# Kernel tuning notes

Measured on AMD Instinct MI355X. Metric: run time of the kernel, lower is better.

The kernel has to match this reference:

```python
import jax, jax.numpy as jnp
import numpy as np

B, S, N, D_IN, D_OUT = 8, 512, 128, 256, 64
D_HID = D_IN // 2


def setup_inputs() -> dict:
    key = jax.random.key(0)
    ks = jax.random.split(key, 12)
    sc_in = 1.0 / np.sqrt(D_IN)
    sc_hid = 1.0 / np.sqrt(D_HID)
    return {
        "x": jax.random.normal(ks[0], (B, S, N, D_IN), jnp.float32),
        "seq_lengths": jax.random.randint(ks[1], (B,), 0, S),
        # attention1: Linear(D_in, D_hid)
        "W1": jax.random.normal(ks[2], (D_HID, D_IN), jnp.float32) * sc_in,
        "b1": jax.random.normal(ks[3], (D_HID,), jnp.float32) * sc_in,
        # weight_len: (D_hid, 1) xavier param, stored as a vector
        "w_len": jax.random.normal(ks[4], (D_HID,), jnp.float32) * sc_hid,
        # attention: Linear(D_in, D_in)
        "Wa": jax.random.normal(ks[5], (D_IN, D_IN), jnp.float32) * sc_in,
        "ba": jax.random.normal(ks[6], (D_IN,), jnp.float32) * sc_in,
        # embedding: Linear(D_in, D_in)
        "We": jax.random.normal(ks[7], (D_IN, D_IN), jnp.float32) * sc_in,
        "be": jax.random.normal(ks[8], (D_IN,), jnp.float32) * sc_in,
        # fc2: Linear(D_in, D_out)
        "Wf": jax.random.normal(ks[9], (D_OUT, D_IN), jnp.float32) * sc_in,
        "bf": jax.random.normal(ks[10], (D_OUT,), jnp.float32) * sc_in,
    }


def reference(x, seq_lengths, W1, b1, w_len, Wa, ba, We, be, Wf, bf):
    # x: (batch, seq_len, num_nodes, D_in) -- torch code transposes to
    # (num_nodes, seq_len, batch, D_in) then loops nodes; vectorized here.
    b, s, n, d = x.shape
    # final_mask = 11 * (pos < length) - 10  -> 1 where valid, -10 where padded
    pos = jnp.arange(s)
    final_mask = jnp.where(pos[None, :] < seq_lengths[:, None], 1.0, -10.0)  # (b, s)
    # per-node length attention with shared weights
    h = jax.nn.relu(jnp.einsum('bsnd,hd->bsnh', x, W1) + b1)       # (b, s, n, hid)
    scores = jnp.einsum('bsnh,h->bsn', h, w_len)                   # (b, s, n)
    scores = scores * final_mask[:, :, None]
    attn = jax.nn.softmax(scores, axis=1)                           # softmax over seq
    pooled = jnp.einsum('bsnd,bsn->bnd', x, attn)                   # (b, n, d)
    # gated readout (dropout is identity in eval)
    att = jax.nn.sigmoid(pooled @ Wa.T + ba)
    emb = jnp.tanh(pooled @ We.T + be)
    g = (att * emb) @ Wf.T + bf                                     # (b, n, D_out)
    m = jnp.max(g, axis=1)
    return jnp.sum(g, axis=1) / n + m
```

## Files before the change

kernel.cpp:

```cpp
#include <hip/hip_runtime.h>
#include <hip/hip_bf16.h>

#define Bb 8
#define Ss 512
#define Nn 128
#define DIN 256
#define DHID 128
#define DOUT 64
#define TN 16
#define TS 32

typedef __attribute__((ext_vector_type(8))) __bf16 bf16x8;
typedef __attribute__((ext_vector_type(4))) __bf16 bf16x4;
typedef __attribute__((ext_vector_type(4))) float f32x4;

__device__ __forceinline__ unsigned short f2bf(float f) {
  unsigned u = __float_as_uint(f);
  u += 0x7fffu + ((u >> 16) & 1u);
  return (unsigned short)(u >> 16);
}
__device__ __forceinline__ float bf2f(unsigned short h) {
  return __uint_as_float(((unsigned)h) << 16);
}

__global__ void prep_w1(const float* __restrict__ W1,
                        unsigned short* __restrict__ w1h,
                        unsigned short* __restrict__ w1l) {
  int i = blockIdx.x * 256 + threadIdx.x;
  float f = W1[i];
  unsigned short h = f2bf(f);
  w1h[i] = h;
  w1l[i] = f2bf(f - bf2f(h));
}

__device__ __forceinline__ void stage4(unsigned short* row, int ci, float4 v) {
  bf16x4 hv, lv;
  hv[0] = (__bf16)v.x; hv[1] = (__bf16)v.y;
  hv[2] = (__bf16)v.z; hv[3] = (__bf16)v.w;
  lv[0] = (__bf16)(v.x - (float)hv[0]);
  lv[1] = (__bf16)(v.y - (float)hv[1]);
  lv[2] = (__bf16)(v.z - (float)hv[2]);
  lv[3] = (__bf16)(v.w - (float)hv[3]);
  *(bf16x4*)(row + ci) = hv;
  *(bf16x4*)(row + 256 + ci) = lv;
}

__global__ __launch_bounds__(512, 4) void flash_kernel(
    const float* __restrict__ x, const unsigned short* __restrict__ w1h,
    const unsigned short* __restrict__ w1l, const float* __restrict__ b1,
    const float* __restrict__ wlen, const int* __restrict__ seqlen,
    float* __restrict__ pml, float* __restrict__ pp) {
  __shared__ __align__(16) unsigned short xs0[TN * 520];
  __shared__ __align__(16) unsigned short xs1[TN * 520];
  __shared__ float part[128];

  const int t = threadIdx.x;
  const int lane = t & 63;
  const int w = t >> 6;
  const int quad = lane >> 4;
  const int l15 = lane & 15;

  const int bi = blockIdx.x;
  const int b = bi >> 7;
  const int ng = (bi >> 4) & 7;
  const int sc = bi & 15;
  const int slen = seqlen[b];

  bf16x8 wh[8], wl8[8];
#pragma unroll
  for (int ks = 0; ks < 8; ++ks) {
    int off = (w * 16 + l15) * 256 + ks * 32 + quad * 8;
    wh[ks] = *(const bf16x8*)(w1h + off);
    wl8[ks] = *(const bf16x8*)(w1l + off);
  }
  const float4 b1q = *(const float4*)(b1 + w * 16 + quad * 4);
  const float4 wlq = *(const float4*)(wlen + w * 16 + quad * 4);

  const int c4 = t & 63;
  const int r1 = w;

  float m1 = -INFINITY, l1 = 0.f, m2 = -INFINITY, l2 = 0.f;
  float4 acc1 = {0.f, 0.f, 0.f, 0.f}, acc2 = {0.f, 0.f, 0.f, 0.f};

  const float4* xbase =
      (const float4*)(x + (((long)b * Ss + sc * TS) * Nn + ng * TN) * DIN);

  unsigned short* xcur = xs0;
  unsigned short* xnxt = xs1;

  float4 cv1 = xbase[t];
  float4 cv2 = xbase[t + 512];
  stage4(xcur + r1 * 520, c4 * 4, cv1);
  stage4(xcur + (r1 + 8) * 520, c4 * 4, cv2);
  __syncthreads();

  for (int i = 0; i < TS; ++i) {
    float4 nv1, nv2;
    const bool more = (i + 1 < TS);
    if (more) {
      const float4* nb = xbase + (long)(i + 1) * (Nn * DIN / 4);
      nv1 = nb[t];
      nv2 = nb[t + 512];
    }

    f32x4 sacc = {0.f, 0.f, 0.f, 0.f};
    const unsigned short* xr = xcur + l15 * 520;
#pragma unroll
    for (int ks = 0; ks < 8; ++ks) {
      const int k0 = ks * 32 + quad * 8;
      bf16x8 ah = *(const bf16x8*)(xr + k0);
      bf16x8 al = *(const bf16x8*)(xr + 256 + k0);
      sacc = __builtin_amdgcn_mfma_f32_16x16x32_bf16(wh[ks], ah, sacc, 0, 0, 0);
      sacc = __builtin_amdgcn_mfma_f32_16x16x32_bf16(wh[ks], al, sacc, 0, 0, 0);
      sacc = __builtin_amdgcn_mfma_f32_16x16x32_bf16(wl8[ks], ah, sacc, 0, 0, 0);
    }
    float p = fmaxf(sacc[0] + b1q.x, 0.f) * wlq.x;
    p = fmaf(fmaxf(sacc[1] + b1q.y, 0.f), wlq.y, p);
    p = fmaf(fmaxf(sacc[2] + b1q.z, 0.f), wlq.z, p);
    p = fmaf(fmaxf(sacc[3] + b1q.w, 0.f), wlq.w, p);
    p += __shfl_xor(p, 16);
    p += __shfl_xor(p, 32);
    if (quad == 0) part[w * 16 + l15] = p;
    __syncthreads();

    float v = part[lane] + part[lane + 64];
    v += __shfl_xor(v, 16);
    v += __shfl_xor(v, 32);
    const int s = sc * TS + i;
    const float mask = (s < slen) ? 1.0f : -10.0f;
    const float s1v = __shfl(v, r1) * mask;
    const float s2v = __shfl(v, r1 + 8) * mask;

    float mn1 = fmaxf(m1, s1v);
    if (mn1 > m1) {
      float a = __expf(m1 - mn1);
      l1 *= a;
      acc1.x *= a; acc1.y *= a; acc1.z *= a; acc1.w *= a;
      m1 = mn1;
    }
    float e1 = __expf(s1v - m1);
    l1 += e1;
    acc1.x = fmaf(e1, cv1.x, acc1.x);
    acc1.y = fmaf(e1, cv1.y, acc1.y);
    acc1.z = fmaf(e1, cv1.z, acc1.z);
    acc1.w = fmaf(e1, cv1.w, acc1.w);

    float mn2 = fmaxf(m2, s2v);
    if (mn2 > m2) {
      float a = __expf(m2 - mn2);
      l2 *= a;
      acc2.x *= a; acc2.y *= a; acc2.z *= a; acc2.w *= a;
      m2 = mn2;
    }
    float e2 = __expf(s2v - m2);
    l2 += e2;
    acc2.x = fmaf(e2, cv2.x, acc2.x);
    acc2.y = fmaf(e2, cv2.y, acc2.y);
    acc2.z = fmaf(e2, cv2.z, acc2.z);
    acc2.w = fmaf(e2, cv2.w, acc2.w);

    if (more) {
      stage4(xnxt + r1 * 520, c4 * 4, nv1);
      stage4(xnxt + (r1 + 8) * 520, c4 * 4, nv2);
      cv1 = nv1;
      cv2 = nv2;
      unsigned short* tmp = xcur; xcur = xnxt; xnxt = tmp;
      __syncthreads();
    }
  }

  float* dst1 = pp + ((long)bi * TN + r1) * 256 + c4 * 4;
  *(float4*)dst1 = acc1;
  float* dst2 = pp + ((long)bi * TN + r1 + 8) * 256 + c4 * 4;
  *(float4*)dst2 = acc2;
  if (lane == 0) {
    pml[bi * 32 + r1] = m1;
    pml[bi * 32 + r1 + 8] = m2;
    pml[bi * 32 + 16 + r1] = l1;
    pml[bi * 32 + 16 + r1 + 8] = l2;
  }
}

__global__ __launch_bounds__(256) void combine_readout(
    const float* __restrict__ pml, const float* __restrict__ pp,
    const float* __restrict__ Wa, const float* __restrict__ ba,
    const float* __restrict__ We, const float* __restrict__ be,
    const float* __restrict__ Wf, const float* __restrict__ bfv,
    float* __restrict__ g) {
  const int bi = blockIdx.x;
  const int b = bi >> 7, n = bi & 127;
  const int ng = n >> 4, nl = n & 15;
  const int t = threadIdx.x;
  __shared__ float coef[16];
  __shared__ __align__(16) float p[256];
  __shared__ __align__(16) float tv[256];

  if (t < 16) {
    const int blk = b * 128 + ng * 16 + t;
    float m = pml[blk * 32 + nl];
    float l = pml[blk * 32 + 16 + nl];
    float M = m;
#pragma unroll
    for (int off = 1; off < 16; off <<= 1) M = fmaxf(M, __shfl_xor(M, off));
    float z = l * expf(m - M);
    float L = z;
#pragma unroll
    for (int off = 1; off < 16; off <<= 1) L += __shfl_xor(L, off);
    coef[t] = expf(m - M) / L;
  }
  __syncthreads();

  float accd = 0.f;
#pragma unroll
  for (int c = 0; c < 16; ++c) {
    accd += coef[c] * pp[((long)(b * 128 + ng * 16 + c) * TN + nl) * 256 + t];
  }
  p[t] = accd;
  __syncthreads();

  float da = ba[t], de = be[t];
  const float4* pa = (const float4*)p;
  const float4* wa = (const float4*)(Wa + (long)t * 256);
  const float4* we = (const float4*)(We + (long)t * 256);
#pragma unroll 4
  for (int i = 0; i < 64; ++i) {
    float4 pv = pa[i], av = wa[i], ev = we[i];
    da += pv.x * av.x + pv.y * av.y + pv.z * av.z + pv.w * av.w;
    de += pv.x * ev.x + pv.y * ev.y + pv.z * ev.z + pv.w * ev.w;
  }
  float sig = 1.0f / (1.0f + expf(-da));
  float th = tanhf(de);
  tv[t] = sig * th;
  __syncthreads();
  if (t < 64) {
    float go = bfv[t];
    const float4* wf = (const float4*)(Wf + (long)t * 256);
    const float4* tp = (const float4*)tv;
#pragma unroll 4
    for (int i = 0; i < 64; ++i) {
      float4 a = tp[i], q = wf[i];
      go += a.x * q.x + a.y * q.y + a.z * q.z + a.w * q.w;
    }
    g[(long)bi * 64 + t] = go;
  }
}

__global__ __launch_bounds__(512) void finalize_kernel(const float* __restrict__ g,
                                                       float* __restrict__ out) {
  const int b = blockIdx.x;
  const int t = threadIdx.x;
  const int o = t & 63, ns = t >> 6;
  float sum = 0.f, mx = -INFINITY;
  for (int n = ns; n < Nn; n += 8) {
    float v = g[((long)b * Nn + n) * DOUT + o];
    sum += v;
    mx = fmaxf(mx, v);
  }
  __shared__ float s1[8][64], s2[8][64];
  s1[ns][o] = sum;
  s2[ns][o] = mx;
  __syncthreads();
  if (ns == 0) {
#pragma unroll
    for (int ww = 1; ww < 8; ++ww) {
      sum += s1[ww][o];
      mx = fmaxf(mx, s2[ww][o]);
    }
    out[b * 64 + o] = sum * (1.0f / 128.0f) + mx;
  }
}

extern "C" void kernel_launch(void* const* d_in, const int* in_sizes, int n_in,
                              void* d_out, int out_size, void* d_ws, size_t ws_size,
                              hipStream_t stream) {
  const float* x   = (const float*)d_in[0];
  const int* seql  = (const int*)d_in[1];
  const float* W1  = (const float*)d_in[2];
  const float* b1  = (const float*)d_in[3];
  const float* wl  = (const float*)d_in[4];
  const float* Wa  = (const float*)d_in[5];
  const float* ba  = (const float*)d_in[6];
  const float* We  = (const float*)d_in[7];
  const float* be  = (const float*)d_in[8];
  const float* Wf  = (const float*)d_in[9];
  const float* bfv = (const float*)d_in[10];
  float* out = (float*)d_out;

  char* ws = (char*)d_ws;
  unsigned short* w1h = (unsigned short*)(ws);
  unsigned short* w1l = (unsigned short*)(ws + 65536);
  float* pml = (float*)(ws + 131072);
  float* pp  = (float*)(ws + 262144);
  float* g   = (float*)(ws + 262144 + 16777216);

  prep_w1<<<128, 256, 0, stream>>>(W1, w1h, w1l);
  flash_kernel<<<1024, 512, 0, stream>>>(x, w1h, w1l, b1, wl, seql, pml, pp);
  combine_readout<<<1024, 256, 0, stream>>>(pml, pp, Wa, ba, We, be, Wf, bfv, g);
  finalize_kernel<<<8, 512, 0, stream>>>(g, out);
}
```

Baseline: 788.9 us.

## Remove per-step barrier in flash loop and batch four nodes per readout block

The flash kernel double-buffers the score partial array and moves the staging of the next x tile ahead of the single barrier, dropping one __syncthreads per sequence step. The combine/readout kernel now handles four nodes per block, so each Wa/We/Wf row load is reused across four pooled vectors and the launch shrinks from 1024 to 256 blocks. This trades fewer barriers and less weight traffic for more registers per thread and fewer readout blocks. Correctness depends on the double-buffered part and xnxt writes not racing with reads from the previous step.

```diff
diff --git a/kernel.cpp b/kernel.cpp
--- a/kernel.cpp
+++ b/kernel.cpp
@@ -52,7 +52,7 @@
     float* __restrict__ pml, float* __restrict__ pp) {
   __shared__ __align__(16) unsigned short xs0[TN * 520];
   __shared__ __align__(16) unsigned short xs1[TN * 520];
-  __shared__ float part[128];
+  __shared__ float part[2][128];
 
   const int t = threadIdx.x;
   const int lane = t & 63;
@@ -94,6 +94,7 @@
   stage4(xcur + (r1 + 8) * 520, c4 * 4, cv2);
   __syncthreads();
 
+  int pb = 0;
   for (int i = 0; i < TS; ++i) {
     float4 nv1, nv2;
     const bool more = (i + 1 < TS);
@@ -120,10 +121,15 @@
     p = fmaf(fmaxf(sacc[3] + b1q.w, 0.f), wlq.w, p);
     p += __shfl_xor(p, 16);
     p += __shfl_xor(p, 32);
-    if (quad == 0) part[w * 16 + l15] = p;
+    if (quad == 0) part[pb][w * 16 + l15] = p;
+
+    if (more) {
+      stage4(xnxt + r1 * 520, c4 * 4, nv1);
+      stage4(xnxt + (r1 + 8) * 520, c4 * 4, nv2);
+    }
     __syncthreads();
 
-    float v = part[lane] + part[lane + 64];
+    float v = part[pb][lane] + part[pb][lane + 64];
     v += __shfl_xor(v, 16);
     v += __shfl_xor(v, 32);
     const int s = sc * TS + i;
@@ -160,13 +166,11 @@
     acc2.w = fmaf(e2, cv2.w, acc2.w);
 
     if (more) {
-      stage4(xnxt + r1 * 520, c4 * 4, nv1);
-      stage4(xnxt + (r1 + 8) * 520, c4 * 4, nv2);
       cv1 = nv1;
       cv2 = nv2;
       unsigned short* tmp = xcur; xcur = xnxt; xnxt = tmp;
-      __syncthreads();
-    }
+    }
+    pb ^= 1;
   }
 
   float* dst1 = pp + ((long)bi * TN + r1) * 256 + c4 * 4;
@@ -188,17 +192,20 @@
     const float* __restrict__ Wf, const float* __restrict__ bfv,
     float* __restrict__ g) {
   const int bi = blockIdx.x;
-  const int b = bi >> 7, n = bi & 127;
-  const int ng = n >> 4, nl = n & 15;
+  const int b = bi >> 5;
+  const int n0 = (bi & 31) * 4;
+  const int ng = n0 >> 4;
+  const int nl0 = n0 & 15;
   const int t = threadIdx.x;
-  __shared__ float coef[16];
-  __shared__ __align__(16) float p[256];
-  __shared__ __align__(16) float tv[256];
-
-  if (t < 16) {
-    const int blk = b * 128 + ng * 16 + t;
-    float m = pml[blk * 32 + nl];
-    float l = pml[blk * 32 + 16 + nl];
+  __shared__ float coef[4][16];
+  __shared__ __align__(16) float p4[4][256];
+  __shared__ __align__(16) float tv4[4][256];
+
+  if (t < 64) {
+    const int j = t >> 4, c = t & 15;
+    const int blk = b * 128 + ng * 16 + c;
+    float m = pml[blk * 32 + nl0 + j];
+    float l = pml[blk * 32 + 16 + nl0 + j];
     float M = m;
 #pragma unroll
     for (int off = 1; off < 16; off <<= 1) M = fmaxf(M, __shfl_xor(M, off));
@@ -206,42 +213,61 @@
     float L = z;
 #pragma unroll
     for (int off = 1; off < 16; off <<= 1) L += __shfl_xor(L, off);
-    coef[t] = expf(m - M) / L;
-  }
-  __syncthreads();
-
-  float accd = 0.f;
-#pragma unroll
+    coef[j][c] = expf(m - M) / L;
+  }
+  __syncthreads();
+
+  float a0 = 0.f, a1 = 0.f, a2 = 0.f, a3 = 0.f;
+#pragma unroll 4
   for (int c = 0; c < 16; ++c) {
-    accd += coef[c] * pp[((long)(b * 128 + ng * 16 + c) * TN + nl) * 256 + t];
-  }
-  p[t] = accd;
-  __syncthreads();
-
-  float da = ba[t], de = be[t];
-  const float4* pa = (const float4*)p;
+    const float* base = pp + ((long)(b * 128 + ng * 16 + c) * TN + nl0) * 256;
+    a0 += coef[0][c] * base[t];
+    a1 += coef[1][c] * base[256 + t];
+    a2 += coef[2][c] * base[512 + t];
+    a3 += coef[3][c] * base[768 + t];
+  }
+  p4[0][t] = a0; p4[1][t] = a1; p4[2][t] = a2; p4[3][t] = a3;
+  __syncthreads();
+
+  const float bat = ba[t], bet = be[t];
+  float da0 = 0.f, da1 = 0.f, da2 = 0.f, da3 = 0.f;
+  float de0 = 0.f, de1 = 0.f, de2 = 0.f, de3 = 0.f;
   const float4* wa = (const float4*)(Wa + (long)t * 256);
   const float4* we = (const float4*)(We + (long)t * 256);
-#pragma unroll 4
+  const float4* q0 = (const float4*)p4[0];
+  const float4* q1 = (const float4*)p4[1];
+  const float4* q2 = (const float4*)p4[2];
+  const float4* q3 = (const float4*)p4[3];
+#pragma unroll 2
   for (int i = 0; i < 64; ++i) {
-    float4 pv = pa[i], av = wa[i], ev = we[i];
-    da += pv.x * av.x + pv.y * av.y + pv.z * av.z + pv.w * av.w;
-    de += pv.x * ev.x + pv.y * ev.y + pv.z * ev.z + pv.w * ev.w;
-  }
-  float sig = 1.0f / (1.0f + expf(-da));
-  float th = tanhf(de);
-  tv[t] = sig * th;
-  __syncthreads();
-  if (t < 64) {
-    float go = bfv[t];
-    const float4* wf = (const float4*)(Wf + (long)t * 256);
-    const float4* tp = (const float4*)tv;
+    float4 av = wa[i], ev = we[i];
+    float4 v0 = q0[i], v1 = q1[i], v2 = q2[i], v3 = q3[i];
+    da0 += v0.x * av.x + v0.y * av.y + v0.z * av.z + v0.w * av.w;
+    de0 += v0.x * ev.x + v0.y * ev.y + v0.z * ev.z + v0.w * ev.w;
+    da1 += v1.x * av.x + v1.y * av.y + v1.z * av.z + v1.w * av.w;
+    de1 += v1.x * ev.x + v1.y * ev.y + v1.z * ev.z + v1.w * ev.w;
+    da2 += v2.x * av.x + v2.y * av.y + v2.z * av.z + v2.w * av.w;
+    de2 += v2.x * ev.x + v2.y * ev.y + v2.z * ev.z + v2.w * ev.w;
+    da3 += v3.x * av.x + v3.y * av.y + v3.z * av.z + v3.w * av.w;
+    de3 += v3.x * ev.x + v3.y * ev.y + v3.z * ev.z + v3.w * ev.w;
+  }
+  tv4[0][t] = (1.0f / (1.0f + expf(-(bat + da0)))) * tanhf(bet + de0);
+  tv4[1][t] = (1.0f / (1.0f + expf(-(bat + da1)))) * tanhf(bet + de1);
+  tv4[2][t] = (1.0f / (1.0f + expf(-(bat + da2)))) * tanhf(bet + de2);
+  tv4[3][t] = (1.0f / (1.0f + expf(-(bat + da3)))) * tanhf(bet + de3);
+  __syncthreads();
+
+  {
+    const int j = t >> 6, o = t & 63;
+    float go = bfv[o];
+    const float4* wf = (const float4*)(Wf + (long)o * 256);
+    const float4* tp = (const float4*)tv4[j];
 #pragma unroll 4
     for (int i = 0; i < 64; ++i) {
       float4 a = tp[i], q = wf[i];
       go += a.x * q.x + a.y * q.y + a.z * q.z + a.w * q.w;
     }
-    g[(long)bi * 64 + t] = go;
+    g[(long)(b * 128 + n0 + j) * 64 + o] = go;
   }
 }
 
@@ -295,6 +321,6 @@
 
   prep_w1<<<128, 256, 0, stream>>>(W1, w1h, w1l);
   flash_kernel<<<1024, 512, 0, stream>>>(x, w1h, w1l, b1, wl, seql, pml, pp);
-  combine_readout<<<1024, 256, 0, stream>>>(pml, pp, Wa, ba, We, be, Wf, bfv, g);
+  combine_readout<<<256, 256, 0, stream>>>(pml, pp, Wa, ba, We, be, Wf, bfv, g);
   finalize_kernel<<<8, 512, 0, stream>>>(g, out);
 }
```

New measurement: 753.0 us. 4.6% less time.
